# Optimization experiments

Hardware: AMD Instinct MI355X
Metric: run time of the kernel (lower is better)

Reference implementation:

```python
import jax, jax.numpy as jnp
import numpy as np

N = 50000          # nodes
E = 800000         # edges (avg degree 16)
DIN, DH, DOUT = 128, 256, 40


def setup_inputs() -> dict:
    key = jax.random.key(0)
    ks = jax.random.split(key, 6)
    x = jax.random.normal(ks[0], (N, DIN), dtype=jnp.float32)
    edge_index = jax.random.randint(ks[1], (2, E), 0, N, dtype=jnp.int32)
    W1 = jax.random.normal(ks[2], (DIN, DH), dtype=jnp.float32) * (1.0 / np.sqrt(DIN))
    b1 = jnp.zeros((DH,), dtype=jnp.float32)
    W2 = jax.random.normal(ks[3], (DH, DOUT), dtype=jnp.float32) * (1.0 / np.sqrt(DH))
    b2 = jnp.zeros((DOUT,), dtype=jnp.float32)
    return {"x": x, "edge_index": edge_index, "W1": W1, "b1": b1, "W2": W2, "b2": b2}


def gcn_conv(x, src, dst, W, b, n):
    # PyG GCNConv: add self-loops, symmetric normalization D^-1/2 A D^-1/2,
    # dense projection, scatter-sum aggregation, then bias.
    deg = jax.ops.segment_sum(jnp.ones_like(dst, dtype=x.dtype), dst, num_segments=n)
    dinv = jnp.where(deg > 0, jax.lax.rsqrt(deg), 0.0)
    norm = dinv[src] * dinv[dst]          # [E+N]
    h = x @ W                              # [N, dout] dense GEMM
    msg = h[src] * norm[:, None]          # gather + scale, [E+N, dout]
    out = jax.ops.segment_sum(msg, dst, num_segments=n)  # scatter-add
    return out + b


def reference(x, edge_index, W1, b1, W2, b2):
    n = x.shape[0]
    loops = jnp.arange(n, dtype=edge_index.dtype)
    src = jnp.concatenate([edge_index[0], loops])
    dst = jnp.concatenate([edge_index[1], loops])
    h = jax.nn.relu(gcn_conv(x, src, dst, W1, b1, n))
    h = gcn_conv(h, src, dst, W2, b2, n)
    return jax.nn.log_softmax(h, axis=1)
```

## Files before the change

### kernel.cpp

```cpp
#include <hip/hip_runtime.h>
#include <math.h>

#define DIN 128
#define DH 256
#define DOUT 40
#define MLP_ROWS 64

#define BSH 7
#define BNODES 128
#define NBUK 391
#define CAP 4096
#define PART_T 512
#define PART_EPB 8
#define PART_CHUNK (PART_T * PART_EPB)

typedef short short8 __attribute__((ext_vector_type(8)));
typedef float f32x4 __attribute__((ext_vector_type(4)));

__device__ inline unsigned f2bf(float f) {
    unsigned u = __float_as_uint(f);
    return (u + 0x7fffu + ((u >> 16) & 1u)) >> 16;
}
__device__ inline float bflo(unsigned u) { return __uint_as_float(u << 16); }
__device__ inline float bfhi(unsigned u) { return __uint_as_float(u & 0xffff0000u); }


__global__ void k_init_cursor(int* __restrict__ gcur) {
    int i = blockIdx.x * blockDim.x + threadIdx.x;
    if (i < NBUK) gcur[i] = i * CAP;
}

__global__ __launch_bounds__(PART_T) void k_partition(
    const int* __restrict__ src, const int* __restrict__ dst,
    int* __restrict__ gcur, unsigned* __restrict__ raw, int E) {
    __shared__ int hist[NBUK];
    __shared__ int lbase[NBUK];
    int tid = threadIdx.x;
    int base_e = blockIdx.x * PART_CHUNK;

    for (int i = tid; i < NBUK; i += PART_T) hist[i] = 0;
    __syncthreads();

    int s[PART_EPB], d[PART_EPB];
#pragma unroll
    for (int k = 0; k < PART_EPB; ++k) {
        int e = base_e + k * PART_T + tid;
        if (e < E) { s[k] = src[e]; d[k] = dst[e]; }
        else d[k] = -1;
    }
#pragma unroll
    for (int k = 0; k < PART_EPB; ++k)
        if (d[k] >= 0) atomicAdd(&hist[d[k] >> BSH], 1);
    __syncthreads();

    for (int b = tid; b < NBUK; b += PART_T) {
        int c = hist[b];
        lbase[b] = c ? atomicAdd(&gcur[b], c) : 0;
    }
    __syncthreads();
    for (int i = tid; i < NBUK; i += PART_T) hist[i] = 0;
    __syncthreads();

#pragma unroll
    for (int k = 0; k < PART_EPB; ++k) {
        if (d[k] >= 0) {
            int b = d[k] >> BSH;
            int pos = lbase[b] + atomicAdd(&hist[b], 1);
            if (pos < (b + 1) * CAP)
                raw[pos] = ((unsigned)(d[k] & (BNODES - 1)) << 16) | (unsigned)s[k];
        }
    }
}

__global__ __launch_bounds__(256) void k_bucket_csr(
    const unsigned* __restrict__ raw, const int* __restrict__ gcur,
    int* __restrict__ row_ptr, int* __restrict__ row_end,
    float* __restrict__ dinv, unsigned short* __restrict__ esrc, int n) {
    __shared__ int cnt[BNODES];
    __shared__ int scn[BNODES];
    __shared__ int lcur[BNODES];
    int b = blockIdx.x;
    int tid = threadIdx.x;
    int base = b * CAP;
    int size = gcur[b] - base;
    if (size > CAP) size = CAP;

    if (tid < BNODES) cnt[tid] = 0;
    __syncthreads();
    for (int i = tid; i < size; i += 256)
        atomicAdd(&cnt[raw[base + i] >> 16], 1);
    __syncthreads();

    if (tid < BNODES) scn[tid] = cnt[tid];
    __syncthreads();
    for (int off = 1; off < BNODES; off <<= 1) {
        int v = 0;
        if (tid < BNODES && tid >= off) v = scn[tid - off];
        __syncthreads();
        if (tid < BNODES) scn[tid] += v;
        __syncthreads();
    }
    if (tid < BNODES) {
        int excl = scn[tid] - cnt[tid];
        lcur[tid] = excl;
        int g = b * BNODES + tid;
        if (g < n) {
            row_ptr[g] = base + excl;
            row_end[g] = base + excl + cnt[tid];
            dinv[g]    = rsqrtf((float)cnt[tid] + 1.0f);
        }
    }
    __syncthreads();
    for (int i = tid; i < size; i += 256) {
        unsigned rec = raw[base + i];
        int pos = atomicAdd(&lcur[rec >> 16], 1);
        esrc[base + pos] = (unsigned short)(rec & 0xffffu);
    }
}


__global__ void k_prep_xb(const float* __restrict__ x, unsigned* __restrict__ xb, int n64) {
    int i = blockIdx.x * blockDim.x + threadIdx.x;
    if (i >= n64) return;
    float2 v = ((const float2*)x)[i];
    xb[i] = f2bf(v.x) | (f2bf(v.y) << 16);
}

__global__ void k_prep_w(const float* __restrict__ W1, const float* __restrict__ W2,
                         unsigned* __restrict__ w1t, unsigned* __restrict__ w2t) {
    int i = blockIdx.x * blockDim.x + threadIdx.x;
    if (i < 256 * 64) {
        int c = i >> 6;
        int kk = (i & 63) * 2;
        w1t[i] = f2bf(W1[kk * DH + c]) | (f2bf(W1[(kk + 1) * DH + c]) << 16);
    } else if (i < 256 * 64 + 48 * 128) {
        int j = i - 256 * 64;
        int col = j >> 7;
        int kk = (j & 127) * 2;
        float a = (col < DOUT) ? W2[kk * DOUT + col] : 0.f;
        float bb = (col < DOUT) ? W2[(kk + 1) * DOUT + col] : 0.f;
        w2t[j] = f2bf(a) | (f2bf(bb) << 16);
    }
}

__global__ void k_gather_agg1(const unsigned* __restrict__ xb,
                              const unsigned short* __restrict__ esrc,
                              const int* __restrict__ row_ptr, const int* __restrict__ row_end,
                              const float* __restrict__ dinv, unsigned* __restrict__ axb, int n) {
    int node = (blockIdx.x * blockDim.x + threadIdx.x) >> 6;
    int lane = threadIdx.x & 63;
    if (node >= n) return;
    int beg = row_ptr[node], end = row_end[node];
    float dn = dinv[node];
    unsigned sv = xb[(size_t)node * 64 + lane];
    float accx = dn * bflo(sv);
    float accy = dn * bfhi(sv);
    int t = beg;
    for (; t + 4 <= end; t += 4) {
        int s0 = esrc[t], s1 = esrc[t + 1], s2 = esrc[t + 2], s3 = esrc[t + 3];
        float w0 = dinv[s0], w1 = dinv[s1], w2 = dinv[s2], w3 = dinv[s3];
        unsigned v0 = xb[(size_t)s0 * 64 + lane];
        unsigned v1 = xb[(size_t)s1 * 64 + lane];
        unsigned v2 = xb[(size_t)s2 * 64 + lane];
        unsigned v3 = xb[(size_t)s3 * 64 + lane];
        accx += w0 * bflo(v0) + w1 * bflo(v1) + w2 * bflo(v2) + w3 * bflo(v3);
        accy += w0 * bfhi(v0) + w1 * bfhi(v1) + w2 * bfhi(v2) + w3 * bfhi(v3);
    }
    for (; t < end; ++t) {
        int s = esrc[t];
        float w = dinv[s];
        unsigned v = xb[(size_t)s * 64 + lane];
        accx += w * bflo(v);
        accy += w * bfhi(v);
    }
    accx *= dn; accy *= dn;
    axb[(size_t)node * 64 + lane] = f2bf(accx) | (f2bf(accy) << 16);
}

__global__ __launch_bounds__(256) void k_mlp_mfma(
    const unsigned short* __restrict__ axb, const unsigned short* __restrict__ w1t,
    const float* __restrict__ b1, const unsigned short* __restrict__ w2t,
    float* __restrict__ p, int n) {
    __shared__ __align__(16) char smem[65536];
    const int tid = threadIdx.x;
    const int lane = tid & 63;
    const int wv = tid >> 6;
    const int l15 = lane & 15;
    const int lg = lane >> 4;
    const int blockRow = blockIdx.x * MLP_ROWS;

    for (int i = tid; i < 256 * 16; i += 256) {
        int j = i >> 4, seg = i & 15;
        short8 v = *(const short8*)(w1t + j * 128 + seg * 8);
        *(short8*)(smem + j * 256 + ((seg * 16) ^ ((j & 7) << 4))) = v;
    }

    int arow = blockRow + wv * 16 + l15;
    if (arow >= n) arow = n - 1;
    const unsigned short* axp = axb + (size_t)arow * DIN + lg * 8;
    short8 aF[4];
#pragma unroll
    for (int ks = 0; ks < 4; ++ks) aF[ks] = *(const short8*)(axp + ks * 32);

    __syncthreads();

    f32x4 acc[16];
#pragma unroll
    for (int nt = 0; nt < 16; ++nt) acc[nt] = (f32x4){0.f, 0.f, 0.f, 0.f};
#pragma unroll
    for (int ks = 0; ks < 4; ++ks) {
        int kb = (ks * 32 + lg * 8) * 2;
#pragma unroll
        for (int nt = 0; nt < 16; ++nt) {
            int j = nt * 16 + l15;
            short8 bF = *(const short8*)(smem + j * 256 + (kb ^ ((j & 7) << 4)));
            acc[nt] = __builtin_amdgcn_mfma_f32_16x16x32_bf16(aF[ks], bF, acc[nt], 0, 0, 0);
        }
    }
    __syncthreads();

    unsigned short* s_h = (unsigned short*)smem;
    unsigned short* s_w2 = (unsigned short*)(smem + 33792);

#pragma unroll
    for (int nt = 0; nt < 16; ++nt) {
        int col = nt * 16 + l15;
        float bias = b1[col];
#pragma unroll
        for (int r = 0; r < 4; ++r) {
            int row = wv * 16 + lg * 4 + r;
            float v = fmaxf(acc[nt][r] + bias, 0.f);
            s_h[row * 264 + col] = (unsigned short)f2bf(v);
        }
    }
    for (int i = tid; i < 48 * 32; i += 256) {
        int j = i >> 5, seg = i & 31;
        short8 v = *(const short8*)(w2t + j * 256 + seg * 8);
        *(short8*)(s_w2 + j * 264 + seg * 8) = v;
    }
    __syncthreads();

    f32x4 acc2[3];
#pragma unroll
    for (int t = 0; t < 3; ++t) acc2[t] = (f32x4){0.f, 0.f, 0.f, 0.f};
#pragma unroll
    for (int ks = 0; ks < 8; ++ks) {
        int k = ks * 32 + lg * 8;
        short8 aH = *(const short8*)(s_h + (wv * 16 + l15) * 264 + k);
#pragma unroll
        for (int t = 0; t < 3; ++t) {
            short8 bF = *(const short8*)(s_w2 + (t * 16 + l15) * 264 + k);
            acc2[t] = __builtin_amdgcn_mfma_f32_16x16x32_bf16(aH, bF, acc2[t], 0, 0, 0);
        }
    }
#pragma unroll
    for (int t = 0; t < 3; ++t) {
        int col = t * 16 + l15;
        if (col < DOUT) {
#pragma unroll
            for (int r = 0; r < 4; ++r) {
                int row = blockRow + wv * 16 + lg * 4 + r;
                if (row < n) p[(size_t)row * DOUT + col] = acc2[t][r];
            }
        }
    }
}

__global__ void k_gather2_lsm(const float* __restrict__ p,
                              const unsigned short* __restrict__ esrc,
                              const int* __restrict__ row_ptr, const int* __restrict__ row_end,
                              const float* __restrict__ dinv, const float* __restrict__ b2,
                              float* __restrict__ out, int n) {
    int node = (blockIdx.x * blockDim.x + threadIdx.x) >> 6;
    int lane = threadIdx.x & 63;
    if (node >= n) return;
    int beg = row_ptr[node], end = row_end[node];
    float dn = dinv[node];
    int cl = (lane < DOUT) ? lane : (DOUT - 1);
    float acc = dn * p[(size_t)node * DOUT + cl];
    int t = beg;
    for (; t + 4 <= end; t += 4) {
        int s0 = esrc[t], s1 = esrc[t + 1], s2 = esrc[t + 2], s3 = esrc[t + 3];
        float w0 = dinv[s0], w1 = dinv[s1], w2 = dinv[s2], w3 = dinv[s3];
        float p0 = p[(size_t)s0 * DOUT + cl];
        float p1 = p[(size_t)s1 * DOUT + cl];
        float p2 = p[(size_t)s2 * DOUT + cl];
        float p3 = p[(size_t)s3 * DOUT + cl];
        acc += w0 * p0 + w1 * p1 + w2 * p2 + w3 * p3;
    }
    for (; t < end; ++t) {
        int s = esrc[t];
        acc += dinv[s] * p[(size_t)s * DOUT + cl];
    }
    float v = (lane < DOUT) ? (dn * acc + b2[lane]) : -INFINITY;
    float m = v;
#pragma unroll
    for (int off = 32; off; off >>= 1) m = fmaxf(m, __shfl_xor(m, off));
    float ex = (lane < DOUT) ? expf(v - m) : 0.f;
    float ssum = ex;
#pragma unroll
    for (int off = 32; off; off >>= 1) ssum += __shfl_xor(ssum, off);
    float ls = logf(ssum);
    if (lane < DOUT) out[(size_t)node * DOUT + lane] = v - m - ls;
}

extern "C" void kernel_launch(void* const* d_in, const int* in_sizes, int n_in,
                              void* d_out, int out_size, void* d_ws, size_t ws_size,
                              hipStream_t stream) {
    const float* x  = (const float*)d_in[0];
    const int*   ei = (const int*)d_in[1];
    const float* W1 = (const float*)d_in[2];
    const float* b1 = (const float*)d_in[3];
    const float* W2 = (const float*)d_in[4];
    const float* b2 = (const float*)d_in[5];
    float* out = (float*)d_out;

    int n = in_sizes[0] / DIN;
    int E = in_sizes[1] / 2;
    const int* src = ei;
    const int* dst = ei + E;

    int*            gcur    = (int*)d_ws;
    int*            row_ptr = gcur + 512;
    int*            row_end = row_ptr + n;
    float*          dinv    = (float*)(row_end + n);
    unsigned*       w1t     = (unsigned*)(dinv + n);
    unsigned*       w2t     = w1t + 16384;
    unsigned*       raw     = w2t + 6144;
    unsigned short* esrc    = (unsigned short*)(raw + (size_t)NBUK * CAP);
    unsigned*       xb      = (unsigned*)(esrc + (size_t)NBUK * CAP);
    unsigned*       axb     = xb + (size_t)n * 64;
    float*          p       = (float*)xb;

    const int B = 256;
    int part_blocks = (E + PART_CHUNK - 1) / PART_CHUNK;

    k_init_cursor<<<(NBUK + B - 1) / B, B, 0, stream>>>(gcur);
    k_partition<<<part_blocks, PART_T, 0, stream>>>(src, dst, gcur, raw, E);
    k_bucket_csr<<<NBUK, B, 0, stream>>>(raw, gcur, row_ptr, row_end, dinv, esrc, n);
    k_prep_xb<<<(n * 64 + B - 1) / B, B, 0, stream>>>(x, xb, n * 64);
    k_prep_w<<<(256 * 64 + 48 * 128 + B - 1) / B, B, 0, stream>>>(W1, W2, w1t, w2t);
    k_gather_agg1<<<(int)(((size_t)n * 64 + B - 1) / B), B, 0, stream>>>(
        xb, esrc, row_ptr, row_end, dinv, axb, n);
    k_mlp_mfma<<<(n + MLP_ROWS - 1) / MLP_ROWS, B, 0, stream>>>(
        (const unsigned short*)axb, (const unsigned short*)w1t, b1,
        (const unsigned short*)w2t, p, n);
    k_gather2_lsm<<<(int)(((size_t)n * 64 + B - 1) / B), B, 0, stream>>>(
        p, esrc, row_ptr, row_end, dinv, b2, out, n);
}
```

Measured before the change: 139.8 us.

## Fuse prep kernels, store layer-2 projection as bf16, unroll gathers by eight

Merges the cursor init, x conversion and weight transposition into one prep kernel, removing two launches. Stores the layer-2 projection p as bf16 instead of fp32, halving the bytes gathered per edge in the second aggregation. Adds an 8-way unrolled edge loop to both gather kernels for more loads in flight. The bf16 p adds rounding error before log_softmax, and the extra unroll raises register use.

New measurement: 124.4 us. -11.0%, faster.

```diff
diff --git a/kernel.cpp b/kernel.cpp
--- a/kernel.cpp
+++ b/kernel.cpp
@@ -23,12 +23,8 @@
 }
 __device__ inline float bflo(unsigned u) { return __uint_as_float(u << 16); }
 __device__ inline float bfhi(unsigned u) { return __uint_as_float(u & 0xffff0000u); }
-
-
-__global__ void k_init_cursor(int* __restrict__ gcur) {
-    int i = blockIdx.x * blockDim.x + threadIdx.x;
-    if (i < NBUK) gcur[i] = i * CAP;
-}
+__device__ inline float bfu(unsigned short u) { return __uint_as_float((unsigned)u << 16); }
+
 
 __global__ __launch_bounds__(PART_T) void k_partition(
     const int* __restrict__ src, const int* __restrict__ dst,
@@ -118,29 +114,34 @@
     }
 }
 
-
-__global__ void k_prep_xb(const float* __restrict__ x, unsigned* __restrict__ xb, int n64) {
+__global__ void k_prep(const float* __restrict__ x, const float* __restrict__ W1,
+                       const float* __restrict__ W2, unsigned* __restrict__ xb,
+                       unsigned* __restrict__ w1t, unsigned* __restrict__ w2t,
+                       int* __restrict__ gcur, int n64) {
     int i = blockIdx.x * blockDim.x + threadIdx.x;
-    if (i >= n64) return;
-    float2 v = ((const float2*)x)[i];
-    xb[i] = f2bf(v.x) | (f2bf(v.y) << 16);
-}
-
-__global__ void k_prep_w(const float* __restrict__ W1, const float* __restrict__ W2,
-                         unsigned* __restrict__ w1t, unsigned* __restrict__ w2t) {
-    int i = blockIdx.x * blockDim.x + threadIdx.x;
+    if (i < n64) {
+        float2 v = ((const float2*)x)[i];
+        xb[i] = f2bf(v.x) | (f2bf(v.y) << 16);
+        return;
+    }
+    i -= n64;
     if (i < 256 * 64) {
         int c = i >> 6;
         int kk = (i & 63) * 2;
         w1t[i] = f2bf(W1[kk * DH + c]) | (f2bf(W1[(kk + 1) * DH + c]) << 16);
-    } else if (i < 256 * 64 + 48 * 128) {
-        int j = i - 256 * 64;
-        int col = j >> 7;
-        int kk = (j & 127) * 2;
+        return;
+    }
+    i -= 256 * 64;
+    if (i < 48 * 128) {
+        int col = i >> 7;
+        int kk = (i & 127) * 2;
         float a = (col < DOUT) ? W2[kk * DOUT + col] : 0.f;
         float bb = (col < DOUT) ? W2[(kk + 1) * DOUT + col] : 0.f;
-        w2t[j] = f2bf(a) | (f2bf(bb) << 16);
-    }
+        w2t[i] = f2bf(a) | (f2bf(bb) << 16);
+        return;
+    }
+    i -= 48 * 128;
+    if (i < NBUK) gcur[i] = i * CAP;
 }
 
 __global__ void k_gather_agg1(const unsigned* __restrict__ xb,
@@ -156,6 +157,24 @@
     float accx = dn * bflo(sv);
     float accy = dn * bfhi(sv);
     int t = beg;
+    for (; t + 8 <= end; t += 8) {
+        int s0 = esrc[t],     s1 = esrc[t + 1], s2 = esrc[t + 2], s3 = esrc[t + 3];
+        int s4 = esrc[t + 4], s5 = esrc[t + 5], s6 = esrc[t + 6], s7 = esrc[t + 7];
+        float w0 = dinv[s0], w1 = dinv[s1], w2 = dinv[s2], w3 = dinv[s3];
+        float w4 = dinv[s4], w5 = dinv[s5], w6 = dinv[s6], w7 = dinv[s7];
+        unsigned v0 = xb[(size_t)s0 * 64 + lane];
+        unsigned v1 = xb[(size_t)s1 * 64 + lane];
+        unsigned v2 = xb[(size_t)s2 * 64 + lane];
+        unsigned v3 = xb[(size_t)s3 * 64 + lane];
+        unsigned v4 = xb[(size_t)s4 * 64 + lane];
+        unsigned v5 = xb[(size_t)s5 * 64 + lane];
+        unsigned v6 = xb[(size_t)s6 * 64 + lane];
+        unsigned v7 = xb[(size_t)s7 * 64 + lane];
+        accx += w0 * bflo(v0) + w1 * bflo(v1) + w2 * bflo(v2) + w3 * bflo(v3)
+              + w4 * bflo(v4) + w5 * bflo(v5) + w6 * bflo(v6) + w7 * bflo(v7);
+        accy += w0 * bfhi(v0) + w1 * bfhi(v1) + w2 * bfhi(v2) + w3 * bfhi(v3)
+              + w4 * bfhi(v4) + w5 * bfhi(v5) + w6 * bfhi(v6) + w7 * bfhi(v7);
+    }
     for (; t + 4 <= end; t += 4) {
         int s0 = esrc[t], s1 = esrc[t + 1], s2 = esrc[t + 2], s3 = esrc[t + 3];
         float w0 = dinv[s0], w1 = dinv[s1], w2 = dinv[s2], w3 = dinv[s3];
@@ -180,7 +199,7 @@
 __global__ __launch_bounds__(256) void k_mlp_mfma(
     const unsigned short* __restrict__ axb, const unsigned short* __restrict__ w1t,
     const float* __restrict__ b1, const unsigned short* __restrict__ w2t,
-    float* __restrict__ p, int n) {
+    unsigned short* __restrict__ pb, int n) {
     __shared__ __align__(16) char smem[65536];
     const int tid = threadIdx.x;
     const int lane = tid & 63;
@@ -260,13 +279,13 @@
 #pragma unroll
             for (int r = 0; r < 4; ++r) {
                 int row = blockRow + wv * 16 + lg * 4 + r;
-                if (row < n) p[(size_t)row * DOUT + col] = acc2[t][r];
+                if (row < n) pb[(size_t)row * DOUT + col] = (unsigned short)f2bf(acc2[t][r]);
             }
         }
     }
 }
 
-__global__ void k_gather2_lsm(const float* __restrict__ p,
+__global__ void k_gather2_lsm(const unsigned short* __restrict__ pb,
                               const unsigned short* __restrict__ esrc,
                               const int* __restrict__ row_ptr, const int* __restrict__ row_end,
                               const float* __restrict__ dinv, const float* __restrict__ b2,
@@ -276,21 +295,37 @@
     if (node >= n) return;
     int beg = row_ptr[node], end = row_end[node];
     float dn = dinv[node];
-    int cl = (lane < DOUT) ? lane : (DOUT - 1);
-    float acc = dn * p[(size_t)node * DOUT + cl];
+    int cl = (lane < DOUT) ? lane : 0;
+    float acc = dn * bfu(pb[(size_t)node * DOUT + cl]);
     int t = beg;
+    for (; t + 8 <= end; t += 8) {
+        int s0 = esrc[t],     s1 = esrc[t + 1], s2 = esrc[t + 2], s3 = esrc[t + 3];
+        int s4 = esrc[t + 4], s5 = esrc[t + 5], s6 = esrc[t + 6], s7 = esrc[t + 7];
+        float w0 = dinv[s0], w1 = dinv[s1], w2 = dinv[s2], w3 = dinv[s3];
+        float w4 = dinv[s4], w5 = dinv[s5], w6 = dinv[s6], w7 = dinv[s7];
+        float p0 = bfu(pb[(size_t)s0 * DOUT + cl]);
+        float p1 = bfu(pb[(size_t)s1 * DOUT + cl]);
+        float p2 = bfu(pb[(size_t)s2 * DOUT + cl]);
+        float p3 = bfu(pb[(size_t)s3 * DOUT + cl]);
+        float p4 = bfu(pb[(size_t)s4 * DOUT + cl]);
+        float p5 = bfu(pb[(size_t)s5 * DOUT + cl]);
+        float p6 = bfu(pb[(size_t)s6 * DOUT + cl]);
+        float p7 = bfu(pb[(size_t)s7 * DOUT + cl]);
+        acc += w0 * p0 + w1 * p1 + w2 * p2 + w3 * p3
+             + w4 * p4 + w5 * p5 + w6 * p6 + w7 * p7;
+    }
     for (; t + 4 <= end; t += 4) {
         int s0 = esrc[t], s1 = esrc[t + 1], s2 = esrc[t + 2], s3 = esrc[t + 3];
         float w0 = dinv[s0], w1 = dinv[s1], w2 = dinv[s2], w3 = dinv[s3];
-        float p0 = p[(size_t)s0 * DOUT + cl];
-        float p1 = p[(size_t)s1 * DOUT + cl];
-        float p2 = p[(size_t)s2 * DOUT + cl];
-        float p3 = p[(size_t)s3 * DOUT + cl];
+        float p0 = bfu(pb[(size_t)s0 * DOUT + cl]);
+        float p1 = bfu(pb[(size_t)s1 * DOUT + cl]);
+        float p2 = bfu(pb[(size_t)s2 * DOUT + cl]);
+        float p3 = bfu(pb[(size_t)s3 * DOUT + cl]);
         acc += w0 * p0 + w1 * p1 + w2 * p2 + w3 * p3;
     }
     for (; t < end; ++t) {
         int s = esrc[t];
-        acc += dinv[s] * p[(size_t)s * DOUT + cl];
+        acc += dinv[s] * bfu(pb[(size_t)s * DOUT + cl]);
     }
     float v = (lane < DOUT) ? (dn * acc + b2[lane]) : -INFINITY;
     float m = v;
@@ -330,21 +365,20 @@
     unsigned short* esrc    = (unsigned short*)(raw + (size_t)NBUK * CAP);
     unsigned*       xb      = (unsigned*)(esrc + (size_t)NBUK * CAP);
     unsigned*       axb     = xb + (size_t)n * 64;
-    float*          p       = (float*)xb;
+    unsigned short* pb      = (unsigned short*)xb;
 
     const int B = 256;
     int part_blocks = (E + PART_CHUNK - 1) / PART_CHUNK;
-
-    k_init_cursor<<<(NBUK + B - 1) / B, B, 0, stream>>>(gcur);
+    int prep_items = n * 64 + 256 * 64 + 48 * 128 + NBUK;
+
+    k_prep<<<(prep_items + B - 1) / B, B, 0, stream>>>(x, W1, W2, xb, w1t, w2t, gcur, n * 64);
     k_partition<<<part_blocks, PART_T, 0, stream>>>(src, dst, gcur, raw, E);
     k_bucket_csr<<<NBUK, B, 0, stream>>>(raw, gcur, row_ptr, row_end, dinv, esrc, n);
-    k_prep_xb<<<(n * 64 + B - 1) / B, B, 0, stream>>>(x, xb, n * 64);
-    k_prep_w<<<(256 * 64 + 48 * 128 + B - 1) / B, B, 0, stream>>>(W1, W2, w1t, w2t);
     k_gather_agg1<<<(int)(((size_t)n * 64 + B - 1) / B), B, 0, stream>>>(
         xb, esrc, row_ptr, row_end, dinv, axb, n);
     k_mlp_mfma<<<(n + MLP_ROWS - 1) / MLP_ROWS, B, 0, stream>>>(
         (const unsigned short*)axb, (const unsigned short*)w1t, b1,
-        (const unsigned short*)w2t, p, n);
+        (const unsigned short*)w2t, pb, n);
     k_gather2_lsm<<<(int)(((size_t)n * 64 + B - 1) / B), B, 0, stream>>>(
-        p, esrc, row_ptr, row_end, dinv, b2, out, n);
-}
+        pb, esrc, row_ptr, row_end, dinv, b2, out, n);
+}
```
